# Optimization experiments

Hardware: AMD Instinct MI355X
Metric: run time of the kernel (lower is better)

## Reference

```python
import jax, jax.numpy as jnp
import numpy as np

B, N, M, K = 8, 24000, 6000, 32
C_IN, C_MID, C_OUT = 64, 128, 256  # channels=[64,128,256]; conv input is C_IN+3 (dp_fj)


def setup_inputs() -> dict:
    key = jax.random.key(0)
    ks = jax.random.split(key, 8)
    return {
        "query_xyz": jax.random.normal(ks[0], (B, M, 3), jnp.float32),
        "support_xyz": jax.random.normal(ks[1], (B, N, 3), jnp.float32),
        "features": jax.random.normal(ks[2], (B, C_IN, N), jnp.float32),
        "neighbor_idx": jax.random.randint(ks[3], (B, M, K), 0, N, dtype=jnp.int32),
        "W1": jax.random.normal(ks[4], (C_MID, C_IN + 3), jnp.float32) * 0.05,
        "b1": jnp.zeros((C_MID,), jnp.float32),
        "W2": jax.random.normal(ks[5], (C_OUT, C_MID), jnp.float32) * 0.05,
        "b2": jnp.zeros((C_OUT,), jnp.float32),
    }


def _conv1d_relu(x, W, b):
    # pointwise conv1d (kernel size 1) + bias + ReLU; x: [B, Cin, N]
    return jax.nn.relu(jnp.einsum('oc,bcn->bon', W, x) + b[None, :, None])


def reference(query_xyz, support_xyz, features, neighbor_idx, W1, b1, W2, b2):
    # Delayed aggregation: transform features FIRST (convs on support points),
    # then gather neighbors per query and max-reduce.
    x = jnp.concatenate([features, support_xyz.transpose(0, 2, 1)], axis=1)  # [B, C_IN+3, N]
    x = _conv1d_relu(x, W1, b1)   # [B, C_MID, N]
    x = _conv1d_relu(x, W2, b2)   # [B, C_OUT, N]
    # grouper: gather neighbor features fj = x[b, :, neighbor_idx[b, m, k]] -> [B, C_OUT, M, K]
    idx = jnp.broadcast_to(neighbor_idx.reshape(B, 1, M * K), (B, C_OUT, M * K))
    fj = jnp.take_along_axis(x, idx, axis=2).reshape(B, C_OUT, M, K)
    # reduction_layer: max over neighbor dim
    return jnp.max(fj, axis=-1)  # [B, C_OUT, M]
```

## Files before the change

kernel.cpp:

```cpp
#include <hip/hip_runtime.h>
#include <hip/hip_bf16.h>

typedef unsigned short u16;
typedef short s16x8 __attribute__((ext_vector_type(8)));
typedef float f32x4 __attribute__((ext_vector_type(4)));
typedef unsigned short u16x8 __attribute__((ext_vector_type(8)));

#define B_   8
#define N_   24000
#define M_   6000
#define K_   32
#define CIN  64
#define CMID 128
#define COUT 256
#define KP1  96
#define QB_  188

__device__ __align__(16) u16 g_W1f[CMID * KP1];
__device__ __align__(16) u16 g_W2f[COUT * CMID];
__device__ __align__(16) u16 g_Yf[(size_t)B_ * N_ * COUT];

__device__ __forceinline__ float bf2f(u16 u) {
    return __uint_as_float(((unsigned)u) << 16);
}
__device__ __forceinline__ u16 f2bf(float f) {
    unsigned u = __float_as_uint(f);
    u += 0x7FFFu + ((u >> 16) & 1u);
    return (u16)(u >> 16);
}
__device__ __forceinline__ unsigned f2bf2(float lo, float hi) {
    __hip_bfloat162 h = __float22bfloat162_rn(make_float2(lo, hi));
    unsigned r;
    __builtin_memcpy(&r, &h, 4);
    return r;
}

__global__ void prep_weights(const float* __restrict__ W1,
                             const float* __restrict__ W2) {
    int t = blockIdx.x * 256 + threadIdx.x;
    if (t < CMID * KP1) {
        int blk = t >> 9, off = t & 511;
        int L = off >> 3, j = off & 7;
        int ln = L & 15, quad = L >> 4;
        int w = blk / 6, r = blk % 6;
        int k0i = r >> 1, mt = r & 1;
        int row = w * 32 + mt * 16 + ln;
        int col = k0i * 32 + quad * 8 + j;
        g_W1f[t] = (col < 67) ? f2bf(W1[row * 67 + col]) : (u16)0;
    } else {
        int i = t - CMID * KP1;
        int blk = i >> 9, off = i & 511;
        int L = off >> 3, j = off & 7;
        int ln = L & 15, quad = L >> 4;
        int w = blk >> 4, r = blk & 15;
        int k0i = r >> 2, mt = r & 3;
        int row = w * 64 + mt * 16 + ln;
        int col = k0i * 32 + quad * 8 + j;
        g_W2f[i] = f2bf(W2[row * 128 + col]);
    }
}

__global__ __launch_bounds__(256) void conv_fused(
        const float* __restrict__ feat, const float* __restrict__ xyz,
        const float* __restrict__ b1,  const float* __restrict__ b2) {
    __shared__ __align__(16) u16 sm[15360];
    u16* Xs = sm;
    u16* Hs = sm + 6656;

    const int tid  = threadIdx.x;
    const int b    = blockIdx.y;
    const int w    = tid >> 6;
    const int L    = tid & 63;
    const int ln   = L & 15;
    const int quad = L >> 4;
    const int p    = L;
    const int cg   = w;

    const float* fbase = feat + (size_t)(b * CIN + cg * 16) * N_;

    float raw[16];
    float px = 0.f, py = 0.f, pz = 0.f;

    {
        const int n0 = blockIdx.x * 192;
#pragma unroll
        for (int jj = 0; jj < 16; ++jj)
            raw[jj] = fbase[(size_t)jj * N_ + n0 + p];
        if (cg == 0) {
            const float* s = xyz + (size_t)(b * N_ + n0 + p) * 3;
            px = s[0]; py = s[1]; pz = s[2];
        }
    }

    for (int t = 0; t < 3; ++t) {
        const int n0 = blockIdx.x * 192 + t * 64;

        {
            u16* dst = Xs + p * 104 + cg * 16;
            uint4 w0, w1;
            w0.x = f2bf2(raw[0],  raw[1]);  w0.y = f2bf2(raw[2],  raw[3]);
            w0.z = f2bf2(raw[4],  raw[5]);  w0.w = f2bf2(raw[6],  raw[7]);
            w1.x = f2bf2(raw[8],  raw[9]);  w1.y = f2bf2(raw[10], raw[11]);
            w1.z = f2bf2(raw[12], raw[13]); w1.w = f2bf2(raw[14], raw[15]);
            *(uint4*)dst = w0;
            *(uint4*)(dst + 8) = w1;
            if (cg == 0) {
                u16* xr = Xs + p * 104 + 64;
                uint4 z4; z4.x = f2bf2(px, py); z4.y = f2bf2(pz, 0.f);
                z4.z = 0u; z4.w = 0u;
                uint4 zz; zz.x = zz.y = zz.z = zz.w = 0u;
                *(uint4*)xr = z4;
                *(uint4*)(xr + 8)  = zz;
                *(uint4*)(xr + 16) = zz;
                *(uint4*)(xr + 24) = zz;
            }
        }
        __syncthreads();

        if (t < 2) {
            const int n1 = n0 + 64;
#pragma unroll
            for (int jj = 0; jj < 16; ++jj)
                raw[jj] = fbase[(size_t)jj * N_ + n1 + p];
            if (cg == 0) {
                const float* s = xyz + (size_t)(b * N_ + n1 + p) * 3;
                px = s[0]; py = s[1]; pz = s[2];
            }
        }

        f32x4 acc1[2][4];
#pragma unroll
        for (int mt = 0; mt < 2; ++mt)
#pragma unroll
            for (int nt = 0; nt < 4; ++nt) {
                f32x4 zz = {0.f, 0.f, 0.f, 0.f};
                acc1[mt][nt] = zz;
            }
#pragma unroll
        for (int k0i = 0; k0i < 3; ++k0i) {
            s16x8 af[2], xf[4];
#pragma unroll
            for (int mt = 0; mt < 2; ++mt)
                af[mt] = *(const s16x8*)(g_W1f + (((w * 3 + k0i) * 2 + mt) << 9) + L * 8);
#pragma unroll
            for (int nt = 0; nt < 4; ++nt)
                xf[nt] = *(const s16x8*)(Xs + (nt * 16 + ln) * 104 + k0i * 32 + quad * 8);
#pragma unroll
            for (int mt = 0; mt < 2; ++mt)
#pragma unroll
                for (int nt = 0; nt < 4; ++nt)
                    acc1[mt][nt] = __builtin_amdgcn_mfma_f32_16x16x32_bf16(
                        af[mt], xf[nt], acc1[mt][nt], 0, 0, 0);
        }
#pragma unroll
        for (int mt = 0; mt < 2; ++mt) {
            int m0 = w * 32 + mt * 16 + quad * 4;
            float4 bv = *(const float4*)(b1 + m0);
#pragma unroll
            for (int nt = 0; nt < 4; ++nt) {
                int pp = nt * 16 + ln;
                uint2 hv;
                hv.x = f2bf2(fmaxf(acc1[mt][nt][0] + bv.x, 0.f),
                             fmaxf(acc1[mt][nt][1] + bv.y, 0.f));
                hv.y = f2bf2(fmaxf(acc1[mt][nt][2] + bv.z, 0.f),
                             fmaxf(acc1[mt][nt][3] + bv.w, 0.f));
                *(uint2*)(Hs + pp * 136 + m0) = hv;
            }
        }
        __syncthreads();

        f32x4 acc2[4][4];
#pragma unroll
        for (int mt = 0; mt < 4; ++mt)
#pragma unroll
            for (int nt = 0; nt < 4; ++nt) {
                f32x4 zz = {0.f, 0.f, 0.f, 0.f};
                acc2[mt][nt] = zz;
            }
#pragma unroll
        for (int k0i = 0; k0i < 4; ++k0i) {
            s16x8 af[4], hf[4];
#pragma unroll
            for (int mt = 0; mt < 4; ++mt)
                af[mt] = *(const s16x8*)(g_W2f + (((w * 4 + k0i) * 4 + mt) << 9) + L * 8);
#pragma unroll
            for (int nt = 0; nt < 4; ++nt)
                hf[nt] = *(const s16x8*)(Hs + (nt * 16 + ln) * 136 + k0i * 32 + quad * 8);
#pragma unroll
            for (int mt = 0; mt < 4; ++mt)
#pragma unroll
                for (int nt = 0; nt < 4; ++nt)
                    acc2[mt][nt] = __builtin_amdgcn_mfma_f32_16x16x32_bf16(
                        af[mt], hf[nt], acc2[mt][nt], 0, 0, 0);
        }

        {
            u16* dstY = g_Yf + ((size_t)b * N_ + n0) * COUT;
#pragma unroll
            for (int mt = 0; mt < 4; ++mt) {
                int c0 = w * 64 + mt * 16 + quad * 4;
                float4 bv = *(const float4*)(b2 + c0);
#pragma unroll
                for (int nt = 0; nt < 4; ++nt) {
                    int pp = nt * 16 + ln;
                    uint2 yv;
                    yv.x = f2bf2(fmaxf(acc2[mt][nt][0] + bv.x, 0.f),
                                 fmaxf(acc2[mt][nt][1] + bv.y, 0.f));
                    yv.y = f2bf2(fmaxf(acc2[mt][nt][2] + bv.z, 0.f),
                                 fmaxf(acc2[mt][nt][3] + bv.w, 0.f));
                    *(uint2*)(dstY + (size_t)pp * COUT + c0) = yv;
                }
            }
        }
    }
}

__global__ __launch_bounds__(256) void gather_max(
        const int* __restrict__ nbr, float* __restrict__ out) {
    __shared__ __align__(16) u16 smem[32 * 400];
    int* sidx  = (int*)smem;
    u16* ssort = smem + 2048;
    int* soff  = (int*)(smem + 3072);
    int* scur  = (int*)(smem + 3328);
    u16* ymax  = smem;

    const int tid = threadIdx.x;
    const int l   = blockIdx.x;
    const int xcd = l & 7;
    const int j   = l >> 3;
    const int cw  = j / QB_;
    const int qb  = j % QB_;
    const int combo = cw * 8 + xcd;
    const int b   = combo >> 2;
    const int q   = combo & 3;
    const int m0  = qb * 32;
    const int row = tid >> 3;
    const int Mv0 = M_ - m0;
    const int Mv  = Mv0 < 32 ? Mv0 : 32;

    if (row < Mv)
        *(int4*)(sidx + tid * 4) =
            *(const int4*)(nbr + ((size_t)b * M_ + m0) * K_ + tid * 4);
    if (tid < 128) scur[tid] = 0;
    __syncthreads();

    unsigned uu[4];
#pragma unroll
    for (int jj = 0; jj < 4; ++jj) {
        unsigned u = (unsigned)sidx[tid * 4 + jj];
        u = u < (unsigned)N_ ? u : 0u;
        uu[jj] = u;
        int pp = (int)(u >> 13);
        if (pp < 2) atomicAdd(&scur[row * 4 + pp], 1);
    }
    __syncthreads();

    if (tid < 32) {
        int c0 = scur[tid * 4 + 0], c1 = scur[tid * 4 + 1];
        soff[tid * 4 + 0] = 0;
        soff[tid * 4 + 1] = c0;
        soff[tid * 4 + 2] = c0 + c1;
        soff[tid * 4 + 3] = 32;
        scur[tid * 4 + 0] = 0;
        scur[tid * 4 + 1] = c0;
        scur[tid * 4 + 2] = c0 + c1;
    }
    __syncthreads();

#pragma unroll
    for (int jj = 0; jj < 4; ++jj) {
        int pp = (int)(uu[jj] >> 13);
        int pos = atomicAdd(&scur[row * 4 + pp], 1);
        ssort[row * 32 + pos] = (u16)uu[jj];
    }
    __syncthreads();

    const int w  = tid >> 6;
    const int L  = tid & 63;
    const int kg = L >> 3;
    const int co = L & 7;
    const u16* base_y = g_Yf + (size_t)b * N_ * COUT + q * 64 + co * 8;

    u16x8 mx[8];
#pragma unroll
    for (int i = 0; i < 8; ++i)
        mx[i] = (u16x8){0, 0, 0, 0, 0, 0, 0, 0};

#pragma unroll
    for (int p = 0; p < 3; ++p) {
#pragma unroll
        for (int h = 0; h < 2; ++h) {
            int mq[4], beg[4], end[4], last[4];
            u16x8 va[4], vb[4];
#pragma unroll
            for (int s = 0; s < 4; ++s) {
                int ml = w * 8 + h * 4 + s;
                mq[s]  = ml < Mv ? ml : 0;
                beg[s] = soff[mq[s] * 4 + p];
                end[s] = soff[mq[s] * 4 + p + 1];
                int lt = end[s] - 1;
                last[s] = lt > 0 ? lt : 0;
                int p0 = beg[s] + kg; p0 = p0 < last[s] ? p0 : last[s];
                unsigned i0 = (unsigned)ssort[mq[s] * 32 + p0];
                va[s] = *(const u16x8*)(base_y + (size_t)i0 * COUT);
            }
#pragma unroll
            for (int s = 0; s < 4; ++s) {
                int p1 = beg[s] + 8 + kg; p1 = p1 < last[s] ? p1 : last[s];
                unsigned i1 = (unsigned)ssort[mq[s] * 32 + p1];
                vb[s] = *(const u16x8*)(base_y + (size_t)i1 * COUT);
            }
#pragma unroll
            for (int s = 0; s < 4; ++s)
                mx[h * 4 + s] = __builtin_elementwise_max(mx[h * 4 + s],
                    __builtin_elementwise_max(va[s], vb[s]));
#pragma unroll
            for (int s = 0; s < 4; ++s) {
                for (int r = beg[s] + 16; r < end[s]; r += 8) {
                    int pq = r + kg; pq = pq < last[s] ? pq : last[s];
                    unsigned ii = (unsigned)ssort[mq[s] * 32 + pq];
                    u16x8 vv = *(const u16x8*)(base_y + (size_t)ii * COUT);
                    mx[h * 4 + s] = __builtin_elementwise_max(mx[h * 4 + s], vv);
                }
            }
        }
    }

    __syncthreads();

#pragma unroll
    for (int i = 0; i < 8; ++i) {
        int ml = w * 8 + i;
        if (ml < Mv) {
            u16x8 m8 = mx[i];
#pragma unroll
            for (int mask = 8; mask <= 32; mask <<= 1) {
                int4 t = *(int4*)&m8;
                t.x = __shfl_xor(t.x, mask);
                t.y = __shfl_xor(t.y, mask);
                t.z = __shfl_xor(t.z, mask);
                t.w = __shfl_xor(t.w, mask);
                m8 = __builtin_elementwise_max(m8, *(u16x8*)&t);
            }
            if (kg == 0)
                *(u16x8*)(ymax + ml * 400 + co * 8) = m8;
        }
    }
    __syncthreads();

    int valid = Mv;
#pragma unroll
    for (int it = 0; it < 2; ++it) {
        int c  = it * 32 + (tid >> 3);
        int mc = (tid & 7) << 2;
        if (mc + 4 <= valid) {
            float4 v;
            v.x = bf2f(ymax[(mc + 0) * 400 + c]);
            v.y = bf2f(ymax[(mc + 1) * 400 + c]);
            v.z = bf2f(ymax[(mc + 2) * 400 + c]);
            v.w = bf2f(ymax[(mc + 3) * 400 + c]);
            *(float4*)(out + (size_t)(b * COUT + q * 64 + c) * M_ + m0 + mc) = v;
        }
    }
}

extern "C" void kernel_launch(void* const* d_in, const int* in_sizes, int n_in,
                              void* d_out, int out_size, void* d_ws, size_t ws_size,
                              hipStream_t stream) {
    const float* xyz  = (const float*)d_in[1];
    const float* feat = (const float*)d_in[2];
    const int*   nbr  = (const int*)d_in[3];
    const float* W1   = (const float*)d_in[4];
    const float* b1   = (const float*)d_in[5];
    const float* W2   = (const float*)d_in[6];
    const float* b2   = (const float*)d_in[7];
    float* out = (float*)d_out;
    (void)d_ws; (void)ws_size;

    prep_weights<<<176, 256, 0, stream>>>(W1, W2);
    conv_fused<<<dim3(125, B_), 256, 0, stream>>>(feat, xyz, b1, b2);
    gather_max<<<32 * QB_, 256, 0, stream>>>(nbr, out);
}
```

Measured before the change: 259.2 us.

## Split conv blocks to one tile each and stage output through swizzled LDS

The conv kernel now gives each block one 64-point tile instead of looping over three with register prefetch, so the grid triples to 375x8 and launch bounds request 5 blocks per SIMD for more occupancy. The bf16 output tile is written to XOR-swizzled shared memory and then stored to global as contiguous 16-byte rows instead of scattered 8-byte stores. This should coalesce writes of the large intermediate buffer. In exchange it drops the software prefetch overlap and adds two barriers per block.

```diff
diff --git a/kernel.cpp b/kernel.cpp
--- a/kernel.cpp
+++ b/kernel.cpp
@@ -60,15 +60,16 @@
     }
 }
 
-__global__ __launch_bounds__(256) void conv_fused(
+__global__ __launch_bounds__(256, 5) void conv_fused(
         const float* __restrict__ feat, const float* __restrict__ xyz,
         const float* __restrict__ b1,  const float* __restrict__ b2) {
-    __shared__ __align__(16) u16 sm[15360];
+    __shared__ __align__(16) u16 sm[16384];
     u16* Xs = sm;
     u16* Hs = sm + 6656;
 
     const int tid  = threadIdx.x;
     const int b    = blockIdx.y;
+    const int n0   = blockIdx.x * 64;
     const int w    = tid >> 6;
     const int L    = tid & 63;
     const int ln   = L & 15;
@@ -76,142 +77,125 @@
     const int p    = L;
     const int cg   = w;
 
-    const float* fbase = feat + (size_t)(b * CIN + cg * 16) * N_;
-
-    float raw[16];
-    float px = 0.f, py = 0.f, pz = 0.f;
-
     {
-        const int n0 = blockIdx.x * 192;
+        const float* fb = feat + (size_t)(b * CIN + cg * 16) * N_ + n0 + p;
+        float r[16];
 #pragma unroll
         for (int jj = 0; jj < 16; ++jj)
-            raw[jj] = fbase[(size_t)jj * N_ + n0 + p];
+            r[jj] = fb[(size_t)jj * N_];
+        u16* dst = Xs + p * 104 + cg * 16;
+        uint4 w0, w1;
+        w0.x = f2bf2(r[0],  r[1]);  w0.y = f2bf2(r[2],  r[3]);
+        w0.z = f2bf2(r[4],  r[5]);  w0.w = f2bf2(r[6],  r[7]);
+        w1.x = f2bf2(r[8],  r[9]);  w1.y = f2bf2(r[10], r[11]);
+        w1.z = f2bf2(r[12], r[13]); w1.w = f2bf2(r[14], r[15]);
+        *(uint4*)dst = w0;
+        *(uint4*)(dst + 8) = w1;
         if (cg == 0) {
             const float* s = xyz + (size_t)(b * N_ + n0 + p) * 3;
-            px = s[0]; py = s[1]; pz = s[2];
-        }
-    }
-
-    for (int t = 0; t < 3; ++t) {
-        const int n0 = blockIdx.x * 192 + t * 64;
-
-        {
-            u16* dst = Xs + p * 104 + cg * 16;
-            uint4 w0, w1;
-            w0.x = f2bf2(raw[0],  raw[1]);  w0.y = f2bf2(raw[2],  raw[3]);
-            w0.z = f2bf2(raw[4],  raw[5]);  w0.w = f2bf2(raw[6],  raw[7]);
-            w1.x = f2bf2(raw[8],  raw[9]);  w1.y = f2bf2(raw[10], raw[11]);
-            w1.z = f2bf2(raw[12], raw[13]); w1.w = f2bf2(raw[14], raw[15]);
-            *(uint4*)dst = w0;
-            *(uint4*)(dst + 8) = w1;
-            if (cg == 0) {
-                u16* xr = Xs + p * 104 + 64;
-                uint4 z4; z4.x = f2bf2(px, py); z4.y = f2bf2(pz, 0.f);
-                z4.z = 0u; z4.w = 0u;
-                uint4 zz; zz.x = zz.y = zz.z = zz.w = 0u;
-                *(uint4*)xr = z4;
-                *(uint4*)(xr + 8)  = zz;
-                *(uint4*)(xr + 16) = zz;
-                *(uint4*)(xr + 24) = zz;
-            }
-        }
-        __syncthreads();
-
-        if (t < 2) {
-            const int n1 = n0 + 64;
-#pragma unroll
-            for (int jj = 0; jj < 16; ++jj)
-                raw[jj] = fbase[(size_t)jj * N_ + n1 + p];
-            if (cg == 0) {
-                const float* s = xyz + (size_t)(b * N_ + n1 + p) * 3;
-                px = s[0]; py = s[1]; pz = s[2];
-            }
-        }
-
-        f32x4 acc1[2][4];
+            u16* xr = Xs + p * 104 + 64;
+            uint4 z4; z4.x = f2bf2(s[0], s[1]); z4.y = f2bf2(s[2], 0.f);
+            z4.z = 0u; z4.w = 0u;
+            uint4 zz; zz.x = zz.y = zz.z = zz.w = 0u;
+            *(uint4*)xr = z4;
+            *(uint4*)(xr + 8)  = zz;
+            *(uint4*)(xr + 16) = zz;
+            *(uint4*)(xr + 24) = zz;
+        }
+    }
+    __syncthreads();
+
+    f32x4 acc1[2][4];
+#pragma unroll
+    for (int mt = 0; mt < 2; ++mt)
+#pragma unroll
+        for (int nt = 0; nt < 4; ++nt) {
+            f32x4 zz = {0.f, 0.f, 0.f, 0.f};
+            acc1[mt][nt] = zz;
+        }
+#pragma unroll
+    for (int k0i = 0; k0i < 3; ++k0i) {
+        s16x8 af[2], xf[4];
 #pragma unroll
         for (int mt = 0; mt < 2; ++mt)
-#pragma unroll
-            for (int nt = 0; nt < 4; ++nt) {
-                f32x4 zz = {0.f, 0.f, 0.f, 0.f};
-                acc1[mt][nt] = zz;
-            }
-#pragma unroll
-        for (int k0i = 0; k0i < 3; ++k0i) {
-            s16x8 af[2], xf[4];
-#pragma unroll
-            for (int mt = 0; mt < 2; ++mt)
-                af[mt] = *(const s16x8*)(g_W1f + (((w * 3 + k0i) * 2 + mt) << 9) + L * 8);
+            af[mt] = *(const s16x8*)(g_W1f + (((w * 3 + k0i) * 2 + mt) << 9) + L * 8);
+#pragma unroll
+        for (int nt = 0; nt < 4; ++nt)
+            xf[nt] = *(const s16x8*)(Xs + (nt * 16 + ln) * 104 + k0i * 32 + quad * 8);
+#pragma unroll
+        for (int mt = 0; mt < 2; ++mt)
 #pragma unroll
             for (int nt = 0; nt < 4; ++nt)
-                xf[nt] = *(const s16x8*)(Xs + (nt * 16 + ln) * 104 + k0i * 32 + quad * 8);
-#pragma unroll
-            for (int mt = 0; mt < 2; ++mt)
-#pragma unroll
-                for (int nt = 0; nt < 4; ++nt)
-                    acc1[mt][nt] = __builtin_amdgcn_mfma_f32_16x16x32_bf16(
-                        af[mt], xf[nt], acc1[mt][nt], 0, 0, 0);
-        }
-#pragma unroll
-        for (int mt = 0; mt < 2; ++mt) {
-            int m0 = w * 32 + mt * 16 + quad * 4;
-            float4 bv = *(const float4*)(b1 + m0);
-#pragma unroll
-            for (int nt = 0; nt < 4; ++nt) {
-                int pp = nt * 16 + ln;
-                uint2 hv;
-                hv.x = f2bf2(fmaxf(acc1[mt][nt][0] + bv.x, 0.f),
-                             fmaxf(acc1[mt][nt][1] + bv.y, 0.f));
-                hv.y = f2bf2(fmaxf(acc1[mt][nt][2] + bv.z, 0.f),
-                             fmaxf(acc1[mt][nt][3] + bv.w, 0.f));
-                *(uint2*)(Hs + pp * 136 + m0) = hv;
-            }
-        }
-        __syncthreads();
-
-        f32x4 acc2[4][4];
+                acc1[mt][nt] = __builtin_amdgcn_mfma_f32_16x16x32_bf16(
+                    af[mt], xf[nt], acc1[mt][nt], 0, 0, 0);
+    }
+#pragma unroll
+    for (int mt = 0; mt < 2; ++mt) {
+        int m0 = w * 32 + mt * 16 + quad * 4;
+        float4 bv = *(const float4*)(b1 + m0);
+#pragma unroll
+        for (int nt = 0; nt < 4; ++nt) {
+            int pp = nt * 16 + ln;
+            uint2 hv;
+            hv.x = f2bf2(fmaxf(acc1[mt][nt][0] + bv.x, 0.f),
+                         fmaxf(acc1[mt][nt][1] + bv.y, 0.f));
+            hv.y = f2bf2(fmaxf(acc1[mt][nt][2] + bv.z, 0.f),
+                         fmaxf(acc1[mt][nt][3] + bv.w, 0.f));
+            *(uint2*)(Hs + pp * 136 + m0) = hv;
+        }
+    }
+    __syncthreads();
+
+    f32x4 acc2[4][4];
+#pragma unroll
+    for (int mt = 0; mt < 4; ++mt)
+#pragma unroll
+        for (int nt = 0; nt < 4; ++nt) {
+            f32x4 zz = {0.f, 0.f, 0.f, 0.f};
+            acc2[mt][nt] = zz;
+        }
+#pragma unroll
+    for (int k0i = 0; k0i < 4; ++k0i) {
+        s16x8 af[4], hf[4];
 #pragma unroll
         for (int mt = 0; mt < 4; ++mt)
-#pragma unroll
-            for (int nt = 0; nt < 4; ++nt) {
-                f32x4 zz = {0.f, 0.f, 0.f, 0.f};
-                acc2[mt][nt] = zz;
-            }
-#pragma unroll
-        for (int k0i = 0; k0i < 4; ++k0i) {
-            s16x8 af[4], hf[4];
-#pragma unroll
-            for (int mt = 0; mt < 4; ++mt)
-                af[mt] = *(const s16x8*)(g_W2f + (((w * 4 + k0i) * 4 + mt) << 9) + L * 8);
+            af[mt] = *(const s16x8*)(g_W2f + (((w * 4 + k0i) * 4 + mt) << 9) + L * 8);
+#pragma unroll
+        for (int nt = 0; nt < 4; ++nt)
+            hf[nt] = *(const s16x8*)(Hs + (nt * 16 + ln) * 136 + k0i * 32 + quad * 8);
+#pragma unroll
+        for (int mt = 0; mt < 4; ++mt)
 #pragma unroll
             for (int nt = 0; nt < 4; ++nt)
-                hf[nt] = *(const s16x8*)(Hs + (nt * 16 + ln) * 136 + k0i * 32 + quad * 8);
-#pragma unroll
-            for (int mt = 0; mt < 4; ++mt)
-#pragma unroll
-                for (int nt = 0; nt < 4; ++nt)
-                    acc2[mt][nt] = __builtin_amdgcn_mfma_f32_16x16x32_bf16(
-                        af[mt], hf[nt], acc2[mt][nt], 0, 0, 0);
-        }
-
-        {
-            u16* dstY = g_Yf + ((size_t)b * N_ + n0) * COUT;
-#pragma unroll
-            for (int mt = 0; mt < 4; ++mt) {
-                int c0 = w * 64 + mt * 16 + quad * 4;
-                float4 bv = *(const float4*)(b2 + c0);
-#pragma unroll
-                for (int nt = 0; nt < 4; ++nt) {
-                    int pp = nt * 16 + ln;
-                    uint2 yv;
-                    yv.x = f2bf2(fmaxf(acc2[mt][nt][0] + bv.x, 0.f),
-                                 fmaxf(acc2[mt][nt][1] + bv.y, 0.f));
-                    yv.y = f2bf2(fmaxf(acc2[mt][nt][2] + bv.z, 0.f),
-                                 fmaxf(acc2[mt][nt][3] + bv.w, 0.f));
-                    *(uint2*)(dstY + (size_t)pp * COUT + c0) = yv;
-                }
-            }
-        }
+                acc2[mt][nt] = __builtin_amdgcn_mfma_f32_16x16x32_bf16(
+                    af[mt], hf[nt], acc2[mt][nt], 0, 0, 0);
+    }
+    __syncthreads();
+
+#pragma unroll
+    for (int mt = 0; mt < 4; ++mt) {
+        int c0 = w * 64 + mt * 16 + quad * 4;
+        float4 bv = *(const float4*)(b2 + c0);
+#pragma unroll
+        for (int nt = 0; nt < 4; ++nt) {
+            int pp = nt * 16 + ln;
+            uint2 yv;
+            yv.x = f2bf2(fmaxf(acc2[mt][nt][0] + bv.x, 0.f),
+                         fmaxf(acc2[mt][nt][1] + bv.y, 0.f));
+            yv.y = f2bf2(fmaxf(acc2[mt][nt][2] + bv.z, 0.f),
+                         fmaxf(acc2[mt][nt][3] + bv.w, 0.f));
+            *(uint2*)(sm + pp * 256 + (c0 ^ ((pp & 31) << 3))) = yv;
+        }
+    }
+    __syncthreads();
+
+    u16* dstY = g_Yf + ((size_t)b * N_ + n0) * COUT;
+#pragma unroll
+    for (int i = 0; i < 8; ++i) {
+        int g = i * 256 + tid;
+        int pp = g >> 5, c16 = g & 31;
+        *(uint4*)(dstY + (size_t)pp * COUT + c16 * 8) =
+            *(const uint4*)(sm + pp * 256 + ((c16 * 8) ^ ((pp & 31) << 3)));
     }
 }
 
@@ -378,6 +362,6 @@
     (void)d_ws; (void)ws_size;
 
     prep_weights<<<176, 256, 0, stream>>>(W1, W2);
-    conv_fused<<<dim3(125, B_), 256, 0, stream>>>(feat, xyz, b1, b2);
+    conv_fused<<<dim3(375, B_), 256, 0, stream>>>(feat, xyz, b1, b2);
     gather_max<<<32 * QB_, 256, 0, stream>>>(nbr, out);
 }
```

Result: slower. 281.8 us (+8.7%).
